# Optimization experiments

Measured on AMD Instinct MI355X. Metric: run time of the kernel, lower is better.

## Reference

```python
import jax, jax.numpy as jnp
import numpy as np

UPDATE_SIZE = 4096
BATCH = 256
NUM_UPDATES = 8
NUM_CH = 2
KEEP = NUM_UPDATES * UPDATE_SIZE                 # 32768
SNAP = (BATCH + NUM_UPDATES - 1) * UPDATE_SIZE   # 1077248


def _window_idx():
    # idx[b, t] = b*update_size + t, the static gather/scatter index pattern
    return jnp.arange(KEEP)[None, :] + (jnp.arange(BATCH) * UPDATE_SIZE)[:, None]  # (B, KEEP)


def _weights(idx):
    # overlap count at each snapshot position, then windowed back: matches
    # torch's scatter(ones).sum(0) followed by window()
    counts = jnp.zeros((SNAP,), jnp.float32).at[idx.reshape(-1)].add(1.0)
    return counts[idx]  # (B, KEEP)


def setup_inputs() -> dict:
    key = jax.random.key(0)
    k1, k2 = jax.random.split(key)
    update = jax.random.normal(k1, (BATCH, NUM_CH, KEEP), dtype=jnp.float32)
    snapshot = jax.random.normal(k2, (NUM_CH, SNAP), dtype=jnp.float32)
    return {"update": update, "snapshot": snapshot}


def reference(update, snapshot):
    idx = _window_idx()                 # (B, KEEP) int32
    weights = _weights(idx)             # (B, KEEP), all >= 1

    # x = update[:, :, -keep:] / num_updates, laid out as (C, B, KEEP)
    x = jnp.transpose(update[:, :, -KEEP:], (1, 0, 2)) / NUM_UPDATES

    # windowed view of the snapshot: windowed[c, b] = snapshot[c, b*US : b*US+KEEP]
    windowed = snapshot[:, idx]         # (C, B, KEEP)
    windowed = windowed / weights[None, :, :] + x

    # scatter-add the weighted windows back into the ring buffer
    # (torch scatters each window into its own zero row then sums over rows;
    #  within a row indices are unique, so this equals a scatter-add)
    acc = jnp.zeros((NUM_CH, SNAP), windowed.dtype).at[:, idx].add(windowed)  # (C, SNAP)

    out_len = BATCH * UPDATE_SIZE
    output = acc[:, :out_len]                    # (C, B*US)
    rest = acc[:, out_len:]                      # (C, (NU-1)*US)
    pad = jnp.zeros((NUM_CH, out_len), acc.dtype)
    new_snapshot = jnp.concatenate([rest, pad], axis=-1)  # (C, SNAP)
    return output[None], new_snapshot
```

## Files before the change

### kernel.cpp

```cpp
#include <hip/hip_runtime.h>

#define UPDATE_SIZE 4096
#define BATCH 256
#define NUM_UPDATES 8
#define NUM_CH 2
#define KEEP (NUM_UPDATES * UPDATE_SIZE)
#define SNAP ((BATCH + NUM_UPDATES - 1) * UPDATE_SIZE)
#define OUT_LEN (BATCH * UPDATE_SIZE)

#define OUT4 (OUT_LEN / 4)
#define SNAP4 (SNAP / 4)
#define REST4 ((SNAP - OUT_LEN) / 4)
#define ROW4 (KEEP / 4)
#define UPD4 (UPDATE_SIZE / 4)
#define TOTAL4 (2 * OUT4 + 2 * SNAP4)

#define KPT 4
#define NTHREADS (TOTAL4 / KPT)

typedef float f32x4 __attribute__((ext_vector_type(4)));

__device__ __forceinline__ f32x4 compute_elem(int idx,
                                              const f32x4* __restrict__ up4,
                                              const f32x4* __restrict__ sn4) {
  int c, s4;
  if (idx < 2 * OUT4) {
    c = idx >> 18;
    s4 = idx & (OUT4 - 1);
  } else {
    const int r = idx - 2 * OUT4;
    c = (r >= SNAP4) ? 1 : 0;
    const int t4 = r - c * SNAP4;
    if (t4 >= REST4) {
      return (f32x4){0.f, 0.f, 0.f, 0.f};
    }
    s4 = OUT4 + t4;
  }

  f32x4 acc = sn4[c * SNAP4 + s4];
  const int q = s4 >> 10;
  if (q >= 7 && q < BATCH) {
    #pragma unroll
    for (int k = 0; k < 8; ++k) {
      const int b = q - 7 + k;
      acc += 0.125f * up4[(b * NUM_CH + c) * ROW4 + (s4 - b * UPD4)];
    }
  } else {
    const int blo = (q >= 7) ? (q - 7) : 0;
    const int bhi = (q < BATCH) ? q : (BATCH - 1);
    for (int b = blo; b <= bhi; ++b) {
      acc += 0.125f * up4[(b * NUM_CH + c) * ROW4 + (s4 - b * UPD4)];
    }
  }
  return acc;
}

__global__ __launch_bounds__(256) void OnlineAverager_62680752718461_kernel(
    const float* __restrict__ update,
    const float* __restrict__ snapshot,
    float* __restrict__ out) {
  const int tid = blockIdx.x * blockDim.x + threadIdx.x;

  const f32x4* __restrict__ up4 = reinterpret_cast<const f32x4*>(update);
  const f32x4* __restrict__ sn4 = reinterpret_cast<const f32x4*>(snapshot);
  f32x4* __restrict__ o4 = reinterpret_cast<f32x4*>(out);

  #pragma unroll
  for (int k = 0; k < KPT; ++k) {
    const int idx = tid + k * NTHREADS;
    const f32x4 acc = compute_elem(idx, up4, sn4);
    __builtin_nontemporal_store(acc, &o4[idx]);
  }
}

extern "C" void kernel_launch(void* const* d_in, const int* in_sizes, int n_in,
                              void* d_out, int out_size, void* d_ws, size_t ws_size,
                              hipStream_t stream) {
  const float* update = (const float*)d_in[0];
  const float* snapshot = (const float*)d_in[1];
  float* out = (float*)d_out;

  const int threads = 256;
  const int blocks = NTHREADS / threads;
  OnlineAverager_62680752718461_kernel<<<blocks, threads, 0, stream>>>(
      update, snapshot, out);
}
```

Baseline: 99.83 us.

## Batch all loads for two elements per thread before reducing, halve work per thread

Each thread now handles two output vectors instead of four. For both elements it issues all 18 global loads (8 update rows plus the snapshot, each) into register arrays before any arithmetic. The sum is then a balanced tree rather than a serial chain. Edge cases are handled with predicated zero loads instead of a variable-length loop. The aim is more memory-level parallelism per thread for this bandwidth-bound gather, at the cost of higher register pressure and twice as many threads.

After: 114.3 us. 14.5% more time.

```diff
diff --git a/kernel.cpp b/kernel.cpp
--- a/kernel.cpp
+++ b/kernel.cpp
@@ -15,15 +15,12 @@
 #define UPD4 (UPDATE_SIZE / 4)
 #define TOTAL4 (2 * OUT4 + 2 * SNAP4)
 
-#define KPT 4
+#define KPT 2
 #define NTHREADS (TOTAL4 / KPT)
 
 typedef float f32x4 __attribute__((ext_vector_type(4)));
 
-__device__ __forceinline__ f32x4 compute_elem(int idx,
-                                              const f32x4* __restrict__ up4,
-                                              const f32x4* __restrict__ sn4) {
-  int c, s4;
+__device__ __forceinline__ void decode(int idx, int& c, int& s4) {
   if (idx < 2 * OUT4) {
     c = idx >> 18;
     s4 = idx & (OUT4 - 1);
@@ -31,28 +28,43 @@
     const int r = idx - 2 * OUT4;
     c = (r >= SNAP4) ? 1 : 0;
     const int t4 = r - c * SNAP4;
-    if (t4 >= REST4) {
-      return (f32x4){0.f, 0.f, 0.f, 0.f};
-    }
-    s4 = OUT4 + t4;
+    s4 = (t4 < REST4) ? (OUT4 + t4) : -1;
   }
+}
 
-  f32x4 acc = sn4[c * SNAP4 + s4];
+__device__ __forceinline__ void issue(int c, int s4,
+                                      const f32x4* __restrict__ up4,
+                                      const f32x4* __restrict__ sn4,
+                                      f32x4* u) {
+  const f32x4 z = {0.f, 0.f, 0.f, 0.f};
+  if (s4 < 0) {
+    #pragma unroll
+    for (int k = 0; k < 9; ++k) u[k] = z;
+    return;
+  }
+  u[8] = sn4[c * SNAP4 + s4];
   const int q = s4 >> 10;
   if (q >= 7 && q < BATCH) {
+    const int base0 = ((q - 7) * NUM_CH + c) * ROW4 + (s4 - (q - 7) * UPD4);
+    #pragma unroll
+    for (int k = 0; k < 8; ++k) {
+      u[k] = up4[base0 + k * (NUM_CH * ROW4 - UPD4)];
+    }
+  } else {
     #pragma unroll
     for (int k = 0; k < 8; ++k) {
       const int b = q - 7 + k;
-      acc += 0.125f * up4[(b * NUM_CH + c) * ROW4 + (s4 - b * UPD4)];
-    }
-  } else {
-    const int blo = (q >= 7) ? (q - 7) : 0;
-    const int bhi = (q < BATCH) ? q : (BATCH - 1);
-    for (int b = blo; b <= bhi; ++b) {
-      acc += 0.125f * up4[(b * NUM_CH + c) * ROW4 + (s4 - b * UPD4)];
+      const bool valid = (b >= 0) && (b < BATCH);
+      u[k] = valid ? up4[(b * NUM_CH + c) * ROW4 + (s4 - b * UPD4)] : z;
     }
   }
-  return acc;
+}
+
+__device__ __forceinline__ f32x4 reduce9(const f32x4* u) {
+  f32x4 s01 = u[0] + u[1], s23 = u[2] + u[3];
+  f32x4 s45 = u[4] + u[5], s67 = u[6] + u[7];
+  f32x4 s = (s01 + s23) + (s45 + s67);
+  return u[8] + 0.125f * s;
 }
 
 __global__ __launch_bounds__(256) void OnlineAverager_62680752718461_kernel(
@@ -65,12 +77,21 @@
   const f32x4* __restrict__ sn4 = reinterpret_cast<const f32x4*>(snapshot);
   f32x4* __restrict__ o4 = reinterpret_cast<f32x4*>(out);
 
-  #pragma unroll
-  for (int k = 0; k < KPT; ++k) {
-    const int idx = tid + k * NTHREADS;
-    const f32x4 acc = compute_elem(idx, up4, sn4);
-    __builtin_nontemporal_store(acc, &o4[idx]);
-  }
+  const int idx0 = tid;
+  const int idx1 = tid + NTHREADS;
+
+  int c0, s40, c1, s41;
+  decode(idx0, c0, s40);
+  decode(idx1, c1, s41);
+
+  f32x4 u0[9], u1[9];
+  issue(c0, s40, up4, sn4, u0);
+  issue(c1, s41, up4, sn4, u1);
+
+  const f32x4 acc0 = reduce9(u0);
+  __builtin_nontemporal_store(acc0, &o4[idx0]);
+  const f32x4 acc1 = reduce9(u1);
+  __builtin_nontemporal_store(acc1, &o4[idx1]);
 }
 
 extern "C" void kernel_launch(void* const* d_in, const int* in_sizes, int n_in,
```
